# Kernel tuning notes

Measured on AMD Instinct MI355X. Metric: run time of the kernel, lower is better.

Reference implementation:

```python
import jax, jax.numpy as jnp
import numpy as np

NUM_CLASSES = 80
ROI_SIZE = 7
SAMPLING = 2          # RoIAlign sampling_ratio
STRIDES = (4, 8, 16, 32)
FINEST_SCALE = 56.0
SCORE_THR = 0.05
IOU_THR = 0.5
MAX_PER_IMG = 100
MEANS = jnp.zeros((4,), jnp.float32)
STDS = jnp.array([0.1, 0.1, 0.2, 0.2], jnp.float32)
MAX_RATIO = abs(float(np.log(16.0 / 1000.0)))


def setup_inputs() -> dict:
    key = jax.random.key(0)
    ks = jax.random.split(key, 20)
    C, H0, W0 = 256, 200, 336
    inp = {}
    for i in range(4):
        inp[f"feat{i}"] = jax.random.normal(ks[i], (1, C, H0 >> i, W0 >> i), jnp.float32)
    N = 1000
    IMG_W, IMG_H = 1344.0, 800.0
    cx = jax.random.uniform(ks[4], (N,), minval=0.0, maxval=IMG_W)
    cy = jax.random.uniform(ks[5], (N,), minval=0.0, maxval=IMG_H)
    w = jax.random.uniform(ks[6], (N,), minval=16.0, maxval=512.0)
    h = jax.random.uniform(ks[7], (N,), minval=16.0, maxval=512.0)
    x1 = jnp.clip(cx - w / 2, 0.0, IMG_W - 1)
    y1 = jnp.clip(cy - h / 2, 0.0, IMG_H - 1)
    x2 = jnp.clip(cx + w / 2, x1 + 1.0, IMG_W)
    y2 = jnp.clip(cy + h / 2, y1 + 1.0, IMG_H)
    inp["proposals"] = jnp.stack([x1, y1, x2, y2], axis=-1)
    D = C * ROI_SIZE * ROI_SIZE  # 12544
    FC = 1024
    inp["fc1_w"] = 0.01 * jax.random.normal(ks[8], (FC, D), jnp.float32)
    inp["fc1_b"] = jnp.zeros((FC,), jnp.float32)
    inp["fc2_w"] = 0.01 * jax.random.normal(ks[9], (FC, FC), jnp.float32)
    inp["fc2_b"] = jnp.zeros((FC,), jnp.float32)
    inp["cls_w"] = 0.01 * jax.random.normal(ks[10], (NUM_CLASSES + 1, FC), jnp.float32)
    inp["cls_b"] = jnp.zeros((NUM_CLASSES + 1,), jnp.float32)
    inp["reg_w"] = 0.01 * jax.random.normal(ks[11], (NUM_CLASSES * 4, FC), jnp.float32)
    inp["reg_b"] = jnp.zeros((NUM_CLASSES * 4,), jnp.float32)
    return inp


def _roi_align(feat, rois, scale):
    # feat [C,H,W]; rois [N,4]; aligned RoIAlign, 7x7 out, sampling_ratio=2
    C, H, W = feat.shape
    P = ROI_SIZE * SAMPLING  # 14 uniform sample points per axis

    def one(roi):
        x1, y1, x2, y2 = roi[0], roi[1], roi[2], roi[3]
        sx = x1 * scale - 0.5
        sy = y1 * scale - 0.5
        rw = (x2 - x1) * scale
        rh = (y2 - y1) * scale
        pts = (jnp.arange(P, dtype=feat.dtype) + 0.5) / P
        xs = sx + pts * rw
        ys = sy + pts * rh
        y0 = jnp.floor(ys)
        x0 = jnp.floor(xs)
        ly = ys - y0
        lx = xs - x0
        y0i = jnp.clip(y0.astype(jnp.int32), 0, H - 1)
        y1i = jnp.clip(y0i + 1, 0, H - 1)
        x0i = jnp.clip(x0.astype(jnp.int32), 0, W - 1)
        x1i = jnp.clip(x0i + 1, 0, W - 1)
        g = lambda yi, xi: feat[:, yi[:, None], xi[None, :]]  # [C,P,P]
        ly_ = ly[None, :, None]
        lx_ = lx[None, None, :]
        val = (1 - ly_) * ((1 - lx_) * g(y0i, x0i) + lx_ * g(y0i, x1i)) \
            + ly_ * ((1 - lx_) * g(y1i, x0i) + lx_ * g(y1i, x1i))
        vy = ((ys >= -1.0) & (ys <= H))[None, :, None]
        vx = ((xs >= -1.0) & (xs <= W))[None, None, :]
        val = jnp.where(vy & vx, val, 0.0)
        # average-pool the 2x2 samples per bin -> [C,7,7]
        return val.reshape(C, ROI_SIZE, SAMPLING, ROI_SIZE, SAMPLING).mean(axis=(2, 4))

    return jax.vmap(one)(rois)  # [N,C,7,7]


def _delta2bbox(proposals, deltas):
    d = deltas.reshape(-1, NUM_CLASSES, 4) * STDS + MEANS
    dx, dy = d[..., 0], d[..., 1]
    dw = jnp.clip(d[..., 2], -MAX_RATIO, MAX_RATIO)
    dh = jnp.clip(d[..., 3], -MAX_RATIO, MAX_RATIO)
    px = ((proposals[:, 0] + proposals[:, 2]) * 0.5)[:, None]
    py = ((proposals[:, 1] + proposals[:, 3]) * 0.5)[:, None]
    pw = (proposals[:, 2] - proposals[:, 0])[:, None]
    ph = (proposals[:, 3] - proposals[:, 1])[:, None]
    gw = pw * jnp.exp(dw)
    gh = ph * jnp.exp(dh)
    gx = px + pw * dx
    gy = py + ph * dy
    return jnp.stack([gx - gw * 0.5, gy - gh * 0.5, gx + gw * 0.5, gy + gh * 0.5], axis=-1)


def _pairwise_iou(b):
    x1, y1, x2, y2 = b[:, 0], b[:, 1], b[:, 2], b[:, 3]
    area = jnp.maximum(x2 - x1, 0.0) * jnp.maximum(y2 - y1, 0.0)
    iw = jnp.maximum(jnp.minimum(x2[:, None], x2[None, :]) - jnp.maximum(x1[:, None], x1[None, :]), 0.0)
    ih = jnp.maximum(jnp.minimum(y2[:, None], y2[None, :]) - jnp.maximum(y1[:, None], y1[None, :]), 0.0)
    inter = iw * ih
    return inter / jnp.maximum(area[:, None] + area[None, :] - inter, 1e-8)


def _nms_one_class(boxes, scores):
    # greedy NMS, static shapes; returns score-sorted boxes/scores + keep mask
    N = scores.shape[0]
    order = jnp.argsort(-scores)
    b = boxes[order]
    s = scores[order]
    iou = _pairwise_iou(b)
    idx = jnp.arange(N)

    def body(i, keep):
        sup = (iou[i] > IOU_THR) & keep[i] & (idx > i)
        return keep & jnp.logical_not(sup)

    keep = jax.lax.fori_loop(0, N, body, s > SCORE_THR)
    return b, s, keep


def _batched_nms(bboxes, scores):
    # bboxes [N,81,4], scores [N,81]; class 80 is background (skipped)
    cls_boxes = jnp.transpose(bboxes[:, :NUM_CLASSES, :], (1, 0, 2))  # [80,N,4]
    cls_scores = scores[:, :NUM_CLASSES].T                            # [80,N]
    b, s, keep = jax.vmap(_nms_one_class)(cls_boxes, cls_scores)
    N = s.shape[1]
    s_flat = jnp.where(keep, s, -1.0).reshape(-1)
    topv, topi = jax.lax.top_k(s_flat, MAX_PER_IMG)
    det_boxes = b.reshape(-1, 4)[topi]
    det_classes = (topi // N).astype(jnp.int32)
    valid = topv > 0.0
    num_det = valid.sum().astype(jnp.int32)
    det_scores = jnp.where(valid, topv, 0.0)
    det_boxes = jnp.where(valid[:, None], det_boxes, 0.0)
    det_classes = jnp.where(valid, det_classes, -1)
    return num_det, det_boxes[None], det_scores[None], det_classes[None]


def _forward(feat0, feat1, feat2, feat3, proposals,
             fc1_w, fc1_b, fc2_w, fc2_b, cls_w, cls_b, reg_w, reg_b):
    feats = [feat0[0], feat1[0], feat2[0], feat3[0]]
    wp = proposals[:, 2] - proposals[:, 0]
    hp = proposals[:, 3] - proposals[:, 1]
    scale = jnp.sqrt(jnp.maximum(wp * hp, 1e-6))
    lvl = jnp.clip(jnp.floor(jnp.log2(scale / FINEST_SCALE + 1e-6)), 0, 3).astype(jnp.int32)
    N = proposals.shape[0]
    C = feats[0].shape[0]
    roi_feats = jnp.zeros((N, C, ROI_SIZE, ROI_SIZE), proposals.dtype)
    for l, stride in enumerate(STRIDES):
        f = _roi_align(feats[l], proposals, 1.0 / stride)
        roi_feats = jnp.where((lvl == l)[:, None, None, None], f, roi_feats)
    h = roi_feats.reshape(N, -1)
    h = jax.nn.relu(h @ fc1_w.T + fc1_b)
    h = jax.nn.relu(h @ fc2_w.T + fc2_b)
    cls_score = h @ cls_w.T + cls_b          # [N,81]
    bbox_pred = h @ reg_w.T + reg_b          # [N,320]
    scores = jax.nn.softmax(cls_score, axis=1)
    boxes = _delta2bbox(proposals, bbox_pred)                          # [N,80,4]
    boxes = jnp.concatenate([boxes, jnp.zeros((N, 1, 4), boxes.dtype)], axis=1)
    return _batched_nms(boxes, scores)


def reference(feat0, feat1, feat2, feat3, proposals,
              fc1_w, fc1_b, fc2_w, fc2_b, cls_w, cls_b, reg_w, reg_b):
    return _forward(feat0, feat1, feat2, feat3, proposals,
                    fc1_w, fc1_b, fc2_w, fc2_b, cls_w, cls_b, reg_w, reg_b)
```

## Files before the change

kernel.cpp:

```cpp
#include <hip/hip_runtime.h>
#include <math.h>

#define NCLS   80
#define NPROP  1000
#define FCDIM  1024
#define DFLAT  12544
#define MPAD   1024
#define MAXR   4.1351665567423560f
#define LDSP   40
#define NMSW   16
#define NCAT   404

#define CSPLIT 8
#define CG     (256 / CSPLIT)

typedef unsigned short ushort_t;
typedef unsigned long long ull_t;
using short8  = __attribute__((ext_vector_type(8))) short;
using float4v = __attribute__((ext_vector_type(4))) float;

__device__ inline ushort_t f2bf(float f) {
    unsigned int u = __float_as_uint(f);
    unsigned int r = (u + 0x7fffu + ((u >> 16) & 1u)) >> 16;
    return (ushort_t)r;
}

__device__ __forceinline__ unsigned cvtpk_bf16(float lo, float hi) {
    unsigned r;
    asm("v_cvt_pk_bf16_f32 %0, %1, %2" : "=v"(r) : "v"(lo), "v"(hi));
    return r;
}

__global__ __launch_bounds__(256) void roi_align_k(
    const float* __restrict__ f0, const float* __restrict__ f1,
    const float* __restrict__ f2, const float* __restrict__ f3,
    const float* __restrict__ props, ushort_t* __restrict__ Abf)
{
    int r  = blockIdx.x;
    int cz = blockIdx.y;
    int t  = threadIdx.x;

    if (r >= NPROP) {
        for (int i = t; i < CG * 49; i += 256)
            Abf[(size_t)r * DFLAT + cz * (CG * 49) + i] = 0;
        return;
    }

    const float4 p = *(const float4*)&props[(size_t)r * 4];
    float wp = p.z - p.x, hp = p.w - p.y;
    float scale = sqrtf(fmaxf(wp * hp, 1e-6f));
    int lvl = (int)floorf(log2f(scale / 56.0f + 1e-6f));
    lvl = min(max(lvl, 0), 3);

    const float* f; int H, W; float sc;
    switch (lvl) {
        case 0:  f = f0; H = 200; W = 336; sc = 0.25f;    break;
        case 1:  f = f1; H = 100; W = 168; sc = 0.125f;   break;
        case 2:  f = f2; H = 50;  W = 84;  sc = 0.0625f;  break;
        default: f = f3; H = 25;  W = 42;  sc = 0.03125f; break;
    }

    if (t >= 196) return;

    int b   = t >> 2;
    int sub = t & 3;
    int by = b / 7, bx = b - by * 7;
    int sy = by * 2 + (sub >> 1);
    int sx = bx * 2 + (sub & 1);

    float startx = p.x * sc - 0.5f, rangex = (p.z - p.x) * sc;
    float starty = p.y * sc - 0.5f, rangey = (p.w - p.y) * sc;
    float posx = startx + (((float)sx + 0.5f) / 14.0f) * rangex;
    float posy = starty + (((float)sy + 0.5f) / 14.0f) * rangey;

    float flx = floorf(posx), fly = floorf(posy);
    float lx = posx - flx, ly = posy - fly;
    int x0 = min(max((int)flx, 0), W - 1);
    int y0 = min(max((int)fly, 0), H - 1);
    int y1 = min(y0 + 1, H - 1);
    bool valid = (posx >= -1.0f) && (posx <= (float)W) &&
                 (posy >= -1.0f) && (posy <= (float)H);
    float vm = valid ? 0.25f : 0.0f;

    float w00 = (1.f - ly) * (1.f - lx) * vm;
    float w01 = (1.f - ly) * lx * vm;
    float w10 = ly * (1.f - lx) * vm;
    float w11 = ly * lx * vm;

    int  xb = min(x0, W - 2);
    bool xr = (x0 == W - 1);
    float wtA = xr ? 0.f : w00, wtB = xr ? (w00 + w01) : w01;
    float wbA = xr ? 0.f : w10, wbB = xr ? (w10 + w11) : w11;
    int ot = y0 * W + xb;
    int ob = y1 * W + xb;

    const int HW = H * W;
    ushort_t* orow = Abf + (size_t)r * DFLAT + cz * (CG * 49);
    const float* pl = f + (size_t)(cz * CG) * HW;

    #pragma unroll 8
    for (int c = 0; c < CG; c++) {
        float2 tv = *(const float2*)(pl + ot);
        float2 bv = *(const float2*)(pl + ob);
        float v = tv.x * wtA + tv.y * wtB + bv.x * wbA + bv.y * wbB;
        v += __shfl_xor(v, 1);
        v += __shfl_xor(v, 2);
        if (sub == 0)
            orow[c * 49 + b] = f2bf(v);
        pl += HW;
    }
}

__global__ __launch_bounds__(256) void gemm_sk_k(
    const ushort_t* __restrict__ A, const float* __restrict__ Wf,
    float* __restrict__ P, int N, int K, int KC)
{
    __shared__ ushort_t As[2][128 * LDSP];
    __shared__ ushort_t Bs[2][128 * LDSP];

    int tid = threadIdx.x;
    int w = tid >> 6, l = tid & 63;
    int wm = (w >> 1) * 64, wn = (w & 1) * 64;

    int bid = (int)blockIdx.x + (int)gridDim.x * ((int)blockIdx.y + (int)gridDim.y * (int)blockIdx.z);
    int bx = bid & 7;
    int slot = bid >> 3;
    int by = slot % (int)gridDim.y;
    int bz = slot / (int)gridDim.y;

    int m0 = by * 128, n0 = bx * 128;
    int kc0 = bz * KC;

    int lrow = tid >> 2;
    int lko  = (tid & 3) * 8;

    const ushort_t* Ag = A  + (size_t)(m0 + lrow) * K + kc0 + lko;
    const float*    Wg = Wf + (size_t)(n0 + lrow) * K + kc0 + lko;
    size_t rowK64 = (size_t)64 * K;

    float4v acc[4][4];
    #pragma unroll
    for (int i = 0; i < 4; i++)
        #pragma unroll
        for (int j = 0; j < 4; j++)
            acc[i][j] = (float4v){0.f, 0.f, 0.f, 0.f};

    int rl = l & 15, q = l >> 4;

    {
        uint4  a0  = *(const uint4*)(Ag);
        uint4  a1  = *(const uint4*)(Ag + rowK64);
        float4 w0a = *(const float4*)(Wg);
        float4 w0b = *(const float4*)(Wg + 4);
        float4 w1a = *(const float4*)(Wg + rowK64);
        float4 w1b = *(const float4*)(Wg + rowK64 + 4);
        uint4 wv0, wv1;
        wv0.x = cvtpk_bf16(w0a.x, w0a.y); wv0.y = cvtpk_bf16(w0a.z, w0a.w);
        wv0.z = cvtpk_bf16(w0b.x, w0b.y); wv0.w = cvtpk_bf16(w0b.z, w0b.w);
        wv1.x = cvtpk_bf16(w1a.x, w1a.y); wv1.y = cvtpk_bf16(w1a.z, w1a.w);
        wv1.z = cvtpk_bf16(w1b.x, w1b.y); wv1.w = cvtpk_bf16(w1b.z, w1b.w);
        *(uint4*)&As[0][lrow * LDSP + lko]        = a0;
        *(uint4*)&As[0][(lrow + 64) * LDSP + lko] = a1;
        *(uint4*)&Bs[0][lrow * LDSP + lko]        = wv0;
        *(uint4*)&Bs[0][(lrow + 64) * LDSP + lko] = wv1;
    }
    __syncthreads();

    int cur = 0;
    for (int k0 = 0; k0 < KC; k0 += 32) {
        bool more = (k0 + 32) < KC;

        uint4 na0, na1;
        float4 nw0a, nw0b, nw1a, nw1b;
        if (more) {
            na0  = *(const uint4*)(Ag + k0 + 32);
            na1  = *(const uint4*)(Ag + rowK64 + k0 + 32);
            nw0a = *(const float4*)(Wg + k0 + 32);
            nw0b = *(const float4*)(Wg + k0 + 36);
            nw1a = *(const float4*)(Wg + rowK64 + k0 + 32);
            nw1b = *(const float4*)(Wg + rowK64 + k0 + 36);
        }

        const ushort_t* Ac = As[cur];
        const ushort_t* Bc = Bs[cur];
        short8 af[4], bfr[4];
        #pragma unroll
        for (int i = 0; i < 4; i++)
            af[i] = *(const short8*)&Ac[(wm + i * 16 + rl) * LDSP + q * 8];
        #pragma unroll
        for (int j = 0; j < 4; j++)
            bfr[j] = *(const short8*)&Bc[(wn + j * 16 + rl) * LDSP + q * 8];

        #pragma unroll
        for (int i = 0; i < 4; i++)
            #pragma unroll
            for (int j = 0; j < 4; j++)
                acc[i][j] = __builtin_amdgcn_mfma_f32_16x16x32_bf16(
                    af[i], bfr[j], acc[i][j], 0, 0, 0);

        if (more) {
            uint4 wv0, wv1;
            wv0.x = cvtpk_bf16(nw0a.x, nw0a.y); wv0.y = cvtpk_bf16(nw0a.z, nw0a.w);
            wv0.z = cvtpk_bf16(nw0b.x, nw0b.y); wv0.w = cvtpk_bf16(nw0b.z, nw0b.w);
            wv1.x = cvtpk_bf16(nw1a.x, nw1a.y); wv1.y = cvtpk_bf16(nw1a.z, nw1a.w);
            wv1.z = cvtpk_bf16(nw1b.x, nw1b.y); wv1.w = cvtpk_bf16(nw1b.z, nw1b.w);
            ushort_t* An = As[cur ^ 1];
            ushort_t* Bn = Bs[cur ^ 1];
            *(uint4*)&An[lrow * LDSP + lko]        = na0;
            *(uint4*)&An[(lrow + 64) * LDSP + lko] = na1;
            *(uint4*)&Bn[lrow * LDSP + lko]        = wv0;
            *(uint4*)&Bn[(lrow + 64) * LDSP + lko] = wv1;
        }

        __syncthreads();
        cur ^= 1;
    }

    float* Pz = P + (size_t)bz * ((size_t)MPAD * N);
    #pragma unroll
    for (int i = 0; i < 4; i++) {
        #pragma unroll
        for (int j = 0; j < 4; j++) {
            int col = n0 + wn + j * 16 + rl;
            #pragma unroll
            for (int rr = 0; rr < 4; rr++) {
                int row = m0 + wm + i * 16 + q * 4 + rr;
                Pz[(size_t)row * N + col] = acc[i][j][rr];
            }
        }
    }
}

__global__ __launch_bounds__(256) void reduce_sk_k(
    const float* __restrict__ P, const float* __restrict__ bias,
    void* __restrict__ Cout, int N, int SK, int relu, int out_bf16)
{
    size_t idx = ((size_t)blockIdx.x * 256 + threadIdx.x) * 4;
    float4 s = *(const float4*)&P[idx];
    for (int z = 1; z < SK; z++) {
        float4 pv = *(const float4*)&P[(size_t)z * ((size_t)MPAD * N) + idx];
        s.x += pv.x; s.y += pv.y; s.z += pv.z; s.w += pv.w;
    }
    int n = (int)(idx % N);
    float4 b = *(const float4*)&bias[n];
    s.x += b.x; s.y += b.y; s.z += b.z; s.w += b.w;
    if (relu) {
        s.x = fmaxf(s.x, 0.f); s.y = fmaxf(s.y, 0.f);
        s.z = fmaxf(s.z, 0.f); s.w = fmaxf(s.w, 0.f);
    }
    if (out_bf16) {
        ushort4 o;
        o.x = f2bf(s.x); o.y = f2bf(s.y); o.z = f2bf(s.z); o.w = f2bf(s.w);
        *(ushort4*)&((ushort_t*)Cout)[idx] = o;
    } else {
        *(float4*)&((float*)Cout)[idx] = s;
    }
}

__global__ __launch_bounds__(256) void concat_w_k(
    const float* __restrict__ reg_w, const float* __restrict__ cls_w,
    const float* __restrict__ reg_b, const float* __restrict__ cls_b,
    float* __restrict__ Wcat, float* __restrict__ bcat)
{
    int row = blockIdx.x;
    int t = threadIdx.x;
    float4 v = make_float4(0.f, 0.f, 0.f, 0.f);
    float bv = 0.f;
    if (row < 320) {
        v = *(const float4*)&reg_w[(size_t)row * FCDIM + t * 4];
        bv = reg_b[row];
    } else if (row < NCAT - 3) {
        v = *(const float4*)&cls_w[(size_t)(row - 320) * FCDIM + t * 4];
        bv = cls_b[row - 320];
    }
    *(float4*)&Wcat[(size_t)row * FCDIM + t * 4] = v;
    if (t == 0) bcat[row] = bv;
}

__global__ __launch_bounds__(256) void gemm_tn_k(
    const float* __restrict__ A, const float* __restrict__ W,
    const float* __restrict__ bias, float* __restrict__ C,
    int M, int N, int K, int relu)
{
    __shared__ float As[16][64];
    __shared__ float Bs[16][64];

    int tid = threadIdx.x;
    int tx = tid & 15;
    int ty = tid >> 4;
    int m0 = blockIdx.y * 64, n0 = blockIdx.x * 64;

    int lr = tid >> 2;
    int lk = (tid & 3) << 2;

    const float* Arow = A + (size_t)(m0 + lr) * K + lk;
    const float* Wrow = W + (size_t)(n0 + lr) * K + lk;
    bool mOK = (m0 + lr) < M;
    bool nOK = (n0 + lr) < N;

    float acc[4][4] = {};

    for (int k0 = 0; k0 < K; k0 += 16) {
        float4 av = mOK ? *(const float4*)(Arow + k0) : make_float4(0.f, 0.f, 0.f, 0.f);
        float4 wv = nOK ? *(const float4*)(Wrow + k0) : make_float4(0.f, 0.f, 0.f, 0.f);
        As[lk + 0][lr] = av.x; As[lk + 1][lr] = av.y;
        As[lk + 2][lr] = av.z; As[lk + 3][lr] = av.w;
        Bs[lk + 0][lr] = wv.x; Bs[lk + 1][lr] = wv.y;
        Bs[lk + 2][lr] = wv.z; Bs[lk + 3][lr] = wv.w;
        __syncthreads();

        #pragma unroll
        for (int kk = 0; kk < 16; kk++) {
            float4 a = *(const float4*)&As[kk][ty << 2];
            float4 b = *(const float4*)&Bs[kk][tx << 2];
            acc[0][0] += a.x * b.x; acc[0][1] += a.x * b.y;
            acc[0][2] += a.x * b.z; acc[0][3] += a.x * b.w;
            acc[1][0] += a.y * b.x; acc[1][1] += a.y * b.y;
            acc[1][2] += a.y * b.z; acc[1][3] += a.y * b.w;
            acc[2][0] += a.z * b.x; acc[2][1] += a.z * b.y;
            acc[2][2] += a.z * b.z; acc[2][3] += a.z * b.w;
            acc[3][0] += a.w * b.x; acc[3][1] += a.w * b.y;
            acc[3][2] += a.w * b.z; acc[3][3] += a.w * b.w;
        }
        __syncthreads();
    }

    #pragma unroll
    for (int i = 0; i < 4; i++) {
        int m = m0 + (ty << 2) + i;
        if (m >= M) continue;
        #pragma unroll
        for (int j = 0; j < 4; j++) {
            int n = n0 + (tx << 2) + j;
            if (n < N) {
                float v = acc[i][j] + bias[n];
                if (relu) v = fmaxf(v, 0.f);
                C[(size_t)m * N + n] = v;
            }
        }
    }
}

__global__ __launch_bounds__(128) void head_post_k(
    const float* __restrict__ hr_s, const float* __restrict__ props,
    float* __restrict__ probsT, float* __restrict__ boxesT)
{
    int r = blockIdx.x, t = threadIdx.x;
    __shared__ float red[128];

    float x = (t < 81) ? hr_s[(size_t)r * NCAT + 320 + t] : -1e30f;
    red[t] = x; __syncthreads();
    for (int s = 64; s > 0; s >>= 1) {
        if (t < s) red[t] = fmaxf(red[t], red[t + s]);
        __syncthreads();
    }
    float mx = red[0];
    __syncthreads();

    float e = (t < 81) ? expf(x - mx) : 0.f;
    red[t] = e; __syncthreads();
    for (int s = 64; s > 0; s >>= 1) {
        if (t < s) red[t] += red[t + s];
        __syncthreads();
    }
    float inv = 1.f / red[0];

    if (t < NCLS) {
        probsT[(size_t)t * NPROP + r] = e * inv;

        const float4 p = *(const float4*)&props[(size_t)r * 4];
        float4 d = *(const float4*)&hr_s[(size_t)r * NCAT + t * 4];
        float dx = d.x * 0.1f, dy = d.y * 0.1f;
        float dw = fminf(fmaxf(d.z * 0.2f, -MAXR), MAXR);
        float dh = fminf(fmaxf(d.w * 0.2f, -MAXR), MAXR);
        float px = (p.x + p.z) * 0.5f, py = (p.y + p.w) * 0.5f;
        float pw = p.z - p.x, ph = p.w - p.y;
        float gw = pw * expf(dw), gh = ph * expf(dh);
        float gx = px + pw * dx, gy = py + ph * dy;
        float4 bo = make_float4(gx - gw * 0.5f, gy - gh * 0.5f,
                                gx + gw * 0.5f, gy + gh * 0.5f);
        *(float4*)&boxesT[(size_t)(t * NPROP + r) * 4] = bo;
    }
}

__global__ __launch_bounds__(512) void sort_k(
    const float* __restrict__ probsT, const float* __restrict__ boxesT,
    float* __restrict__ sortedS, float* __restrict__ sortedB)
{
    int c = blockIdx.x, t = threadIdx.x;
    __shared__ float sk[1024];
    __shared__ int   si[1024];

    for (int j = t; j < 1024; j += 512) {
        sk[j] = (j < NPROP) ? probsT[(size_t)c * NPROP + j] : -1e30f;
        si[j] = j;
    }
    __syncthreads();

    for (int size = 2; size <= 1024; size <<= 1) {
        for (int stride = size >> 1; stride > 0; stride >>= 1) {
            int i = (t << 1) - (t & (stride - 1));
            int j = i + stride;
            float ka = sk[i], kb = sk[j];
            int ia = si[i], ib = si[j];
            bool aFirst = (ka > kb) || (ka == kb && ia < ib);
            bool desc = ((i & size) == 0);
            if (desc ? !aFirst : aFirst) {
                sk[i] = kb; sk[j] = ka; si[i] = ib; si[j] = ia;
            }
            __syncthreads();
        }
    }

    for (int j = t; j < NPROP; j += 512) {
        sortedS[(size_t)c * NPROP + j] = sk[j];
        const float4 bb = *(const float4*)&boxesT[(size_t)(c * NPROP + si[j]) * 4];
        *(float4*)&sortedB[(size_t)(c * NPROP + j) * 4] = bb;
    }
}

__global__ __launch_bounds__(256) void nms_k(
    const float* __restrict__ sortedS, const float* __restrict__ sortedB,
    ull_t* __restrict__ masks, float* __restrict__ candS, int* __restrict__ candI)
{
    int c = blockIdx.x, t = threadIdx.x;
    __shared__ float x1s[NPROP], y1s[NPROP], x2s[NPROP], y2s[NPROP], ars[NPROP];
    __shared__ unsigned char kp[NPROP];
    __shared__ int segc[256];

    for (int j = t; j < NPROP; j += 256) {
        float4 b = *(const float4*)&sortedB[(size_t)(c * NPROP + j) * 4];
        x1s[j] = b.x; y1s[j] = b.y; x2s[j] = b.z; y2s[j] = b.w;
        ars[j] = fmaxf(b.z - b.x, 0.f) * fmaxf(b.w - b.y, 0.f);
        kp[j] = sortedS[(size_t)c * NPROP + j] > 0.05f ? 1 : 0;
    }
    __syncthreads();

    ull_t* M = masks + (size_t)c * NPROP * NMSW;
    for (int i = t; i < NPROP; i += 256) {
        if (!kp[i]) continue;
        float xi1 = x1s[i], yi1 = y1s[i], xi2 = x2s[i], yi2 = y2s[i], ai = ars[i];
        for (int w = 0; w < NMSW; w++) {
            ull_t m = 0ull;
            int j0 = w << 6;
            #pragma unroll 4
            for (int k = 0; k < 64; k++) {
                int j = j0 + k;
                if (j < NPROP) {
                    float iw = fmaxf(fminf(xi2, x2s[j]) - fmaxf(xi1, x1s[j]), 0.f);
                    float ih = fmaxf(fminf(yi2, y2s[j]) - fmaxf(yi1, y1s[j]), 0.f);
                    float inter = iw * ih;
                    float iou = inter / fmaxf(ai + ars[j] - inter, 1e-8f);
                    if (iou > 0.5f) m |= (1ull << k);
                }
            }
            M[(size_t)i * NMSW + w] = m;
        }
    }
    __syncthreads();

    if (t < 64) {
        ull_t rem = 0ull;
        for (int i = 0; i < NPROP; i++) {
            if (kp[i]) {
                ull_t w = __shfl(rem, i >> 6);
                if ((w >> (i & 63)) & 1ull) {
                    if (t == 0) kp[i] = 0;
                } else {
                    if (t < NMSW) rem |= M[(size_t)i * NMSW + t];
                }
            }
        }
    }
    __syncthreads();

    int j0 = t * 4;
    int cnt = 0;
    #pragma unroll
    for (int k = 0; k < 4; k++) {
        int j = j0 + k;
        if (j < NPROP && kp[j]) cnt++;
    }
    segc[t] = cnt;
    __syncthreads();
    for (int off = 1; off < 256; off <<= 1) {
        int add = (t >= off) ? segc[t - off] : 0;
        __syncthreads();
        segc[t] += add;
        __syncthreads();
    }
    int pos = segc[t] - cnt;
    #pragma unroll
    for (int k = 0; k < 4; k++) {
        int j = j0 + k;
        if (j < NPROP && kp[j]) {
            if (pos < 100) {
                candS[c * 100 + pos] = sortedS[(size_t)c * NPROP + j];
                candI[c * 100 + pos] = c * NPROP + j;
            }
            pos++;
        }
    }
    int total = segc[255];
    for (int p = total + t; p < 100; p += 256) {
        candS[c * 100 + p] = -2e30f;
        candI[c * 100 + p] = 0x7fffffff;
    }
}

__global__ __launch_bounds__(256) void merge_k(
    const float* __restrict__ candS, const int* __restrict__ candI,
    const float* __restrict__ sortedB, float* __restrict__ out)
{
    int t = threadIdx.x;
    __shared__ float cs[NCLS * 101];
    __shared__ int   ci[NCLS * 101];
    __shared__ float topv[100];
    __shared__ int   topi[100];

    for (int i = t; i < NCLS * 100; i += 256) {
        int c = i / 100, j = i - c * 100;
        cs[c * 101 + j] = candS[i];
        ci[c * 101 + j] = candI[i];
    }
    __syncthreads();

    if (t < 64) {
        int h1 = 0, h2 = 0;
        int c2 = t + 64;
        for (int r = 0; r < 100; r++) {
            float v = -2e30f; int fi = 0x7fffffff; int cls = 0;
            if (h1 < 100) { v = cs[t * 101 + h1]; fi = ci[t * 101 + h1]; cls = t; }
            if (c2 < NCLS && h2 < 100) {
                float v2 = cs[c2 * 101 + h2]; int fi2 = ci[c2 * 101 + h2];
                if (v2 > v || (v2 == v && fi2 < fi)) { v = v2; fi = fi2; cls = c2; }
            }
            #pragma unroll
            for (int s = 1; s < 64; s <<= 1) {
                float ov = __shfl_xor(v, s);
                int ofi  = __shfl_xor(fi, s);
                int ocl  = __shfl_xor(cls, s);
                if (ov > v || (ov == v && ofi < fi)) { v = ov; fi = ofi; cls = ocl; }
            }
            if (t == 0) { topv[r] = v; topi[r] = fi; }
            if (cls == t) h1++;
            else if (c2 < NCLS && cls == c2) h2++;
        }
    }
    __syncthreads();

    if (t < 100) {
        float v = topv[t]; int fi = topi[t];
        bool valid = v > 0.0f;
        float4 bb = make_float4(0.f, 0.f, 0.f, 0.f);
        if (valid) bb = *(const float4*)&sortedB[(size_t)fi * 4];
        out[1 + t * 4 + 0] = bb.x;
        out[1 + t * 4 + 1] = bb.y;
        out[1 + t * 4 + 2] = bb.z;
        out[1 + t * 4 + 3] = bb.w;
        out[401 + t] = valid ? v : 0.0f;
        out[501 + t] = valid ? (float)(fi / NPROP) : -1.0f;
    }
    if (t == 0) {
        int n = 0;
        for (int r = 0; r < 100; r++) n += (topv[r] > 0.0f) ? 1 : 0;
        out[0] = (float)n;
    }
}

extern "C" void kernel_launch(void* const* d_in, const int* in_sizes, int n_in,
                              void* d_out, int out_size, void* d_ws, size_t ws_size,
                              hipStream_t stream)
{
    const float* f0    = (const float*)d_in[0];
    const float* f1    = (const float*)d_in[1];
    const float* f2    = (const float*)d_in[2];
    const float* f3    = (const float*)d_in[3];
    const float* props = (const float*)d_in[4];
    const float* fc1_w = (const float*)d_in[5];
    const float* fc1_b = (const float*)d_in[6];
    const float* fc2_w = (const float*)d_in[7];
    const float* fc2_b = (const float*)d_in[8];
    const float* cls_w = (const float*)d_in[9];
    const float* cls_b = (const float*)d_in[10];
    const float* reg_w = (const float*)d_in[11];
    const float* reg_b = (const float*)d_in[12];
    float* out = (float*)d_out;

    unsigned char* base = (unsigned char*)d_ws;
    ushort_t* Abf  = (ushort_t*)(base);
    ushort_t* h1   = (ushort_t*)(base + 25690112);
    float*    P1   = (float*)(base + 27787264);
    float*    P2   = (float*)(base + 27787264);
    float*    h2   = (float*)(base + 44564480);
    float*    hr_s    = (float*)(base + 48758784);
    float*    probsT  = (float*)(base + 50401280);
    float*    boxesT  = (float*)(base + 50721280);
    float*    sortedS = (float*)(base + 52001280);
    float*    sortedB = (float*)(base + 52321280);
    float*    candS   = (float*)(base + 53601280);
    int*      candI   = (int*)(base + 53633280);
    float*    Wcat    = (float*)(base + 53665280);
    float*    bcat    = (float*)(base + 55320064);
    ull_t*    masks   = (ull_t*)(base);

    roi_align_k<<<dim3(MPAD, CSPLIT), 256, 0, stream>>>(f0, f1, f2, f3, props, Abf);

    gemm_sk_k<<<dim3(FCDIM / 128, MPAD / 128, 8), 256, 0, stream>>>(
        Abf, fc1_w, P1, FCDIM, DFLAT, DFLAT / 8);
    reduce_sk_k<<<(MPAD * FCDIM / 4) / 256, 256, 0, stream>>>(
        P1, fc1_b, h1, FCDIM, 8, 1, 1);

    concat_w_k<<<NCAT, 256, 0, stream>>>(reg_w, cls_w, reg_b, cls_b, Wcat, bcat);

    gemm_sk_k<<<dim3(FCDIM / 128, MPAD / 128, 4), 256, 0, stream>>>(
        h1, fc2_w, P2, FCDIM, FCDIM, FCDIM / 4);
    reduce_sk_k<<<(MPAD * FCDIM / 4) / 256, 256, 0, stream>>>(
        P2, fc2_b, h2, FCDIM, 4, 1, 0);

    gemm_tn_k<<<dim3((NCAT + 63) / 64, (NPROP + 63) / 64), 256, 0, stream>>>(
        h2, Wcat, bcat, hr_s, NPROP, NCAT, FCDIM, 0);

    head_post_k<<<NPROP, 128, 0, stream>>>(hr_s, props, probsT, boxesT);
    sort_k<<<NCLS, 512, 0, stream>>>(probsT, boxesT, sortedS, sortedB);
    nms_k<<<NCLS, 256, 0, stream>>>(sortedS, sortedB, masks, candS, candI);
    merge_k<<<1, 256, 0, stream>>>(candS, candI, sortedB, out);
}
```

Measured before the change: 544.9 us.

## Pack sort keys into 64-bit words, double channel split, simplify merge load

The bitonic sort now packs an order-preserving float score and an inverted index into a single 64-bit key. Each compare-exchange then needs one comparison and two shared-memory swaps instead of separate float and index arrays. The RoIAlign channel split goes from 8 to 16, so more blocks with fewer channels each run in parallel. The merge kernel's candidate load now assigns classes to wavefronts, which drops the integer division per element. Ties in the sort still resolve toward the lower index.

```diff
diff --git a/kernel.cpp b/kernel.cpp
--- a/kernel.cpp
+++ b/kernel.cpp
@@ -11,7 +11,7 @@
 #define NMSW   16
 #define NCAT   404
 
-#define CSPLIT 8
+#define CSPLIT 16
 #define CG     (256 / CSPLIT)
 
 typedef unsigned short ushort_t;
@@ -29,6 +29,15 @@
     unsigned r;
     asm("v_cvt_pk_bf16_f32 %0, %1, %2" : "=v"(r) : "v"(lo), "v"(hi));
     return r;
+}
+
+__device__ __forceinline__ unsigned ordf(float f) {
+    unsigned u = __float_as_uint(f);
+    return (u & 0x80000000u) ? ~u : (u | 0x80000000u);
+}
+__device__ __forceinline__ float iordf(unsigned k) {
+    unsigned u = (k & 0x80000000u) ? (k & 0x7FFFFFFFu) : ~k;
+    return __uint_as_float(u);
 }
 
 __global__ __launch_bounds__(256) void roi_align_k(
@@ -388,12 +397,11 @@
     float* __restrict__ sortedS, float* __restrict__ sortedB)
 {
     int c = blockIdx.x, t = threadIdx.x;
-    __shared__ float sk[1024];
-    __shared__ int   si[1024];
+    __shared__ ull_t skk[1024];
 
     for (int j = t; j < 1024; j += 512) {
-        sk[j] = (j < NPROP) ? probsT[(size_t)c * NPROP + j] : -1e30f;
-        si[j] = j;
+        float s = (j < NPROP) ? probsT[(size_t)c * NPROP + j] : -1e30f;
+        skk[j] = ((ull_t)ordf(s) << 32) | (ull_t)(0x7FFFFFFFu - (unsigned)j);
     }
     __syncthreads();
 
@@ -401,20 +409,21 @@
         for (int stride = size >> 1; stride > 0; stride >>= 1) {
             int i = (t << 1) - (t & (stride - 1));
             int j = i + stride;
-            float ka = sk[i], kb = sk[j];
-            int ia = si[i], ib = si[j];
-            bool aFirst = (ka > kb) || (ka == kb && ia < ib);
+            ull_t ka = skk[i], kb = skk[j];
+            bool aFirst = ka > kb;
             bool desc = ((i & size) == 0);
             if (desc ? !aFirst : aFirst) {
-                sk[i] = kb; sk[j] = ka; si[i] = ib; si[j] = ia;
+                skk[i] = kb; skk[j] = ka;
             }
             __syncthreads();
         }
     }
 
     for (int j = t; j < NPROP; j += 512) {
-        sortedS[(size_t)c * NPROP + j] = sk[j];
-        const float4 bb = *(const float4*)&boxesT[(size_t)(c * NPROP + si[j]) * 4];
+        ull_t k = skk[j];
+        int idx = (int)(0x7FFFFFFFu - (unsigned)(k & 0xFFFFFFFFull));
+        sortedS[(size_t)c * NPROP + j] = iordf((unsigned)(k >> 32));
+        const float4 bb = *(const float4*)&boxesT[(size_t)(c * NPROP + idx) * 4];
         *(float4*)&sortedB[(size_t)(c * NPROP + j) * 4] = bb;
     }
 }
@@ -518,10 +527,14 @@
     __shared__ float topv[100];
     __shared__ int   topi[100];
 
-    for (int i = t; i < NCLS * 100; i += 256) {
-        int c = i / 100, j = i - c * 100;
-        cs[c * 101 + j] = candS[i];
-        ci[c * 101 + j] = candI[i];
+    {
+        int wv = t >> 6, ln = t & 63;
+        for (int c = wv; c < NCLS; c += 4) {
+            for (int j = ln; j < 100; j += 64) {
+                cs[c * 101 + j] = candS[c * 100 + j];
+                ci[c * 101 + j] = candI[c * 100 + j];
+            }
+        }
     }
     __syncthreads();
 
```

Result: no change. 546.1 us (+0.2%).
